# Kernel optimization log

Measured on AMD Instinct MI355X. Metric: run time of the kernel, lower is better.

The kernel has to match this reference:

```python
import jax, jax.numpy as jnp
import numpy as np
from jax import lax

B, T, D = 1, 2048, 2048
H, KVH, HD = 16, 4, 128
BETA = 0.9
ROPE_BASE = 10000.0


def _causal_prefix_ema(x, beta):
    # x: (B, T, D); m_t = beta * m_{t-1} + (1 - beta) * x_t, m_{-1} = 0
    def step(m, xt):
        m = beta * m + (1.0 - beta) * xt
        return m, m
    _, ys = lax.scan(step, jnp.zeros_like(x[:, 0]), jnp.swapaxes(x, 0, 1))
    return jnp.swapaxes(ys, 0, 1)


def _rotate_half(x):
    x1, x2 = jnp.split(x, 2, axis=-1)
    return jnp.concatenate([-x2, x1], axis=-1)


def _rope_cos_sin(t, hd, dtype):
    inv_freq = 1.0 / (ROPE_BASE ** (jnp.arange(0, hd, 2, dtype=jnp.float32) / hd))
    freqs = jnp.arange(t, dtype=jnp.float32)[:, None] * inv_freq[None, :]  # (T, HD/2)
    emb = jnp.concatenate([freqs, freqs], axis=-1)  # (T, HD)
    return jnp.cos(emb).astype(dtype)[None, None], jnp.sin(emb).astype(dtype)[None, None]


def setup_inputs() -> dict:
    key = jax.random.key(0)
    ks = jax.random.split(key, 8)
    std = 0.02
    return {
        "hidden_states": jax.random.normal(ks[0], (B, T, D), jnp.float32),
        "Wq": jax.random.normal(ks[1], (D, H * HD), jnp.float32) * std,
        "Wk": jax.random.normal(ks[2], (D, KVH * HD), jnp.float32) * std,
        "Wv": jax.random.normal(ks[3], (D, KVH * HD), jnp.float32) * std,
        "Wo": jax.random.normal(ks[4], (H * HD, D), jnp.float32) * std,
        "Wr1": jax.random.normal(ks[5], (D, D // 2), jnp.float32) * std,
        "br1": jnp.zeros((D // 2,), jnp.float32),
        "Wr2": jax.random.normal(ks[6], (D // 2, 2), jnp.float32) * std,
        "br2": jnp.zeros((2,), jnp.float32),
    }


def reference(hidden_states, Wq, Wk, Wv, Wo, Wr1, br1, Wr2, br2):
    b, t, d = hidden_states.shape
    q = hidden_states @ Wq  # (B, T, H*HD)

    # multi-level memories: l1 = raw, l2 = causal prefix EMA
    l2 = _causal_prefix_ema(hidden_states, BETA)

    # router MLP on q + softmax over levels
    h = jax.nn.silu(q @ Wr1 + br1)
    lam = jax.nn.softmax(h @ Wr2 + br2, axis=-1)  # (B, T, 2)
    fused = lam[..., 0:1] * hidden_states + lam[..., 1:2] * l2

    # shape to heads
    q_s = q.reshape(b, t, H, HD).transpose(0, 2, 1, 3)                 # (B, H, T, HD)
    k_s = (fused @ Wk).reshape(b, t, KVH, HD).transpose(0, 2, 1, 3)    # (B, KVH, T, HD)
    v_s = (fused @ Wv).reshape(b, t, KVH, HD).transpose(0, 2, 1, 3)

    # RoPE
    cos, sin = _rope_cos_sin(t, HD, q_s.dtype)
    q_s = q_s * cos + _rotate_half(q_s) * sin
    k_s = k_s * cos + _rotate_half(k_s) * sin

    # repeat kv for GQA
    n_rep = H // KVH
    k_s = jnp.repeat(k_s, n_rep, axis=1)
    v_s = jnp.repeat(v_s, n_rep, axis=1)

    # causal SDPA
    scale = 1.0 / jnp.sqrt(jnp.asarray(HD, q_s.dtype))
    scores = jnp.einsum("bhqd,bhkd->bhqk", q_s, k_s) * scale
    causal = jnp.tril(jnp.ones((t, t), dtype=bool))
    scores = jnp.where(causal[None, None], scores, jnp.finfo(scores.dtype).min)
    attn = jax.nn.softmax(scores, axis=-1)
    out = jnp.einsum("bhqk,bhkd->bhqd", attn, v_s)  # (B, H, T, HD)

    out = out.transpose(0, 2, 1, 3).reshape(b, t, H * HD)
    return out @ Wo
```

## Files before the change

### kernel.cpp

```cpp
#include <hip/hip_runtime.h>
#include <hip/hip_bf16.h>

#define T_SEQ 2048
#define D_MODEL 2048
#define NH 16
#define NKVH 4
#define HD 128

typedef __attribute__((ext_vector_type(8))) short bf16x8;
typedef __attribute__((ext_vector_type(4))) float f32x4;

static __device__ __forceinline__ short f32_to_bf16(float f) {
    unsigned u = __float_as_uint(f);
    u += 0x7fffu + ((u >> 16) & 1u);
    return (short)(u >> 16);
}
static __device__ __forceinline__ float bf16_to_f32(short s) {
    return __uint_as_float(((unsigned)(unsigned short)s) << 16);
}
static __device__ __forceinline__ void gl_to_lds16(const void* g, void* l) {
    __builtin_amdgcn_global_load_lds(
        (const __attribute__((address_space(1))) unsigned int*)g,
        (__attribute__((address_space(3))) unsigned int*)l, 16, 0, 0);
}

template<int BM>
__global__ __launch_bounds__(256) void gemm_bt_kernel(
    const short* __restrict__ A, const short* __restrict__ Bt,
    float* __restrict__ Cf, short* __restrict__ Cb,
    int M, int N, int K, const float* __restrict__ bias, int act)
{
    constexpr int NI = (BM == 128) ? 4 : 2;
    constexpr int ACH = BM / 32;
    __shared__ short Alds[2][BM * 64];
    __shared__ short Blds[2][128 * 64];

    const int tid = threadIdx.x;
    const int wave = tid >> 6, lane = tid & 63;
    const int l16 = lane & 15, quad = lane >> 4;
    const int wm = (BM == 128) ? (wave >> 1) * 64 : 0;
    const int wn = (BM == 128) ? (wave & 1) * 64 : wave * 32;
    const int m0 = blockIdx.y * BM, n0 = blockIdx.x * 128;
    const int niter = K >> 6;

    f32x4 acc[4][NI] = {};

    #pragma unroll
    for (int p = 0; p < ACH; ++p) {
        int li = p * 256 + tid;
        int row = li >> 3, sc = li & 7;
        gl_to_lds16(A + (size_t)(m0 + row) * K + ((sc ^ (row & 7)) * 8),
                    &Alds[0][(size_t)(p * 256 + wave * 64) * 8]);
    }
    #pragma unroll
    for (int p = 0; p < 4; ++p) {
        int li = p * 256 + tid;
        int row = li >> 3, sc = li & 7;
        gl_to_lds16(Bt + (size_t)(n0 + row) * K + ((sc ^ (row & 7)) * 8),
                    &Blds[0][(size_t)(p * 256 + wave * 64) * 8]);
    }

    for (int t = 0; t < niter; ++t) {
        asm volatile("s_waitcnt vmcnt(0)\n\ts_barrier" ::: "memory");

        if (t + 1 < niter) {
            int k1 = (t + 1) << 6;
            int nb = (t + 1) & 1;
            #pragma unroll
            for (int p = 0; p < ACH; ++p) {
                int li = p * 256 + tid;
                int row = li >> 3, sc = li & 7;
                gl_to_lds16(A + (size_t)(m0 + row) * K + k1 + ((sc ^ (row & 7)) * 8),
                            &Alds[nb][(size_t)(p * 256 + wave * 64) * 8]);
            }
            #pragma unroll
            for (int p = 0; p < 4; ++p) {
                int li = p * 256 + tid;
                int row = li >> 3, sc = li & 7;
                gl_to_lds16(Bt + (size_t)(n0 + row) * K + k1 + ((sc ^ (row & 7)) * 8),
                            &Blds[nb][(size_t)(p * 256 + wave * 64) * 8]);
            }
        }

        const short* Ab = Alds[t & 1];
        const short* Bb = Blds[t & 1];
        #pragma unroll
        for (int kk = 0; kk < 2; ++kk) {
            bf16x8 a[4], b[NI];
            #pragma unroll
            for (int i = 0; i < 4; ++i)
                a[i] = *(const bf16x8*)
                    &Ab[(size_t)(wm + i * 16 + l16) * 64 + (((kk * 4 + quad) ^ (l16 & 7)) * 8)];
            #pragma unroll
            for (int i = 0; i < NI; ++i)
                b[i] = *(const bf16x8*)
                    &Bb[(size_t)(wn + i * 16 + l16) * 64 + (((kk * 4 + quad) ^ (l16 & 7)) * 8)];
            #pragma unroll
            for (int mi = 0; mi < 4; ++mi)
                #pragma unroll
                for (int ni = 0; ni < NI; ++ni)
                    acc[mi][ni] = __builtin_amdgcn_mfma_f32_16x16x32_bf16(
                        a[mi], b[ni], acc[mi][ni], 0, 0, 0);
        }
    }

    #pragma unroll
    for (int mi = 0; mi < 4; ++mi) {
        #pragma unroll
        for (int ni = 0; ni < NI; ++ni) {
            int col = n0 + wn + ni * 16 + l16;
            float bv = bias ? bias[col] : 0.0f;
            #pragma unroll
            for (int r = 0; r < 4; ++r) {
                int row = m0 + wm + mi * 16 + quad * 4 + r;
                float x = acc[mi][ni][r] + bv;
                if (act) x = x / (1.0f + __expf(-x));
                size_t o = (size_t)row * N + col;
                if (Cf) Cf[o] = x;
                if (Cb) Cb[o] = f32_to_bf16(x);
            }
        }
    }
}

__global__ __launch_bounds__(256) void transpose_all_kernel(
    const float* __restrict__ Wq, const float* __restrict__ Wk,
    const float* __restrict__ Wv, const float* __restrict__ Wr1,
    const float* __restrict__ Wo, short* __restrict__ Wq_t,
    short* __restrict__ Wkv_t, short* __restrict__ Wr1_t,
    short* __restrict__ Wo_t)
{
    __shared__ float tile[32][33];
    int bx = blockIdx.x;
    const float* src; short* dst; int ld, cb;
    if (bx < 64)       { src = Wq;  dst = Wq_t;  ld = 2048; cb = bx; }
    else if (bx < 80)  { src = Wk;  dst = Wkv_t; ld = 512;  cb = bx - 64; }
    else if (bx < 96)  { src = Wv;  dst = Wkv_t + (size_t)512 * 2048; ld = 512; cb = bx - 80; }
    else if (bx < 128) { src = Wr1; dst = Wr1_t; ld = 1024; cb = bx - 96; }
    else               { src = Wo;  dst = Wo_t;  ld = 2048; cb = bx - 128; }
    int c0 = cb * 32, r0 = blockIdx.y * 32;
    int t = threadIdx.x;
    int r = t >> 3, c4 = (t & 7) * 4;
    float4 v = *(const float4*)&src[(size_t)(r0 + r) * ld + c0 + c4];
    tile[r][c4 + 0] = v.x; tile[r][c4 + 1] = v.y;
    tile[r][c4 + 2] = v.z; tile[r][c4 + 3] = v.w;
    __syncthreads();
    short o[4];
    #pragma unroll
    for (int j = 0; j < 4; ++j) o[j] = f32_to_bf16(tile[c4 + j][r]);
    *(uint2*)&dst[(size_t)(c0 + r) * 2048 + r0 + c4] = *(const uint2*)o;
}

__global__ __launch_bounds__(256) void transpose_bf_kernel(
    const short* __restrict__ src, int ld, short* __restrict__ dst, int ldd)
{
    __shared__ float tile[32][33];
    int r0 = blockIdx.y * 32, c0 = blockIdx.x * 32;
    int x = threadIdx.x & 31, y = threadIdx.x >> 5;
    #pragma unroll
    for (int i = 0; i < 4; ++i)
        tile[y + i * 8][x] = bf16_to_f32(src[(size_t)(r0 + y + i * 8) * ld + c0 + x]);
    __syncthreads();
    #pragma unroll
    for (int i = 0; i < 4; ++i)
        dst[(size_t)(c0 + y + i * 8) * ldd + r0 + x] = f32_to_bf16(tile[x][y + i * 8]);
}

__global__ void conv_bf16_kernel(const float* __restrict__ src, short* __restrict__ dst)
{
    int i = blockIdx.x * blockDim.x + threadIdx.x;
    float4 v = ((const float4*)src)[i];
    short o[4] = {f32_to_bf16(v.x), f32_to_bf16(v.y), f32_to_bf16(v.z), f32_to_bf16(v.w)};
    *(uint2*)(dst + (size_t)i * 4) = *(const uint2*)o;
}

__global__ __launch_bounds__(256) void ema_kernel(const float* __restrict__ hs,
                                                  float* __restrict__ l2)
{
    int d = blockIdx.y * 256 + threadIdx.x;
    int t0 = blockIdx.x * 128;
    int ts = t0 - 192; if (ts < 0) ts = 0;
    float m = 0.0f;
    for (int tb = ts; tb < t0; tb += 16) {
        float buf[16];
        #pragma unroll
        for (int j = 0; j < 16; ++j) buf[j] = hs[(size_t)(tb + j) * D_MODEL + d];
        #pragma unroll
        for (int j = 0; j < 16; ++j) m = 0.9f * m + 0.1f * buf[j];
    }
    for (int tb = t0; tb < t0 + 128; tb += 16) {
        float buf[16];
        #pragma unroll
        for (int j = 0; j < 16; ++j) buf[j] = hs[(size_t)(tb + j) * D_MODEL + d];
        #pragma unroll
        for (int j = 0; j < 16; ++j) { m = 0.9f * m + 0.1f * buf[j]; buf[j] = m; }
        #pragma unroll
        for (int j = 0; j < 16; ++j) l2[(size_t)(tb + j) * D_MODEL + d] = buf[j];
    }
}

__global__ __launch_bounds__(64) void lam_kernel(
    const short* __restrict__ h, const float* __restrict__ Wr2,
    const float* __restrict__ br2, float* __restrict__ lam)
{
    int t = blockIdx.x;
    int lane = threadIdx.x;
    float z0 = 0.0f, z1 = 0.0f;
    for (int i = lane; i < 1024; i += 64) {
        float hv = bf16_to_f32(h[(size_t)t * 1024 + i]);
        z0 += hv * Wr2[i * 2 + 0];
        z1 += hv * Wr2[i * 2 + 1];
    }
    #pragma unroll
    for (int off = 1; off < 64; off <<= 1) {
        z0 += __shfl_xor(z0, off);
        z1 += __shfl_xor(z1, off);
    }
    if (lane == 0) {
        z0 += br2[0]; z1 += br2[1];
        float mx = fmaxf(z0, z1);
        float e0 = expf(z0 - mx), e1 = expf(z1 - mx);
        float inv = 1.0f / (e0 + e1);
        lam[t * 2 + 0] = e0 * inv;
        lam[t * 2 + 1] = e1 * inv;
    }
}

__global__ void fuse_kernel(const float* __restrict__ hs, const float* __restrict__ l2,
                            const float* __restrict__ lam, short* __restrict__ fused)
{
    int idx = blockIdx.x * blockDim.x + threadIdx.x;
    int t = idx >> 9;
    float a0 = lam[t * 2 + 0], a1 = lam[t * 2 + 1];
    float4 a = ((const float4*)hs)[idx];
    float4 b = ((const float4*)l2)[idx];
    short o[4] = {f32_to_bf16(a0 * a.x + a1 * b.x), f32_to_bf16(a0 * a.y + a1 * b.y),
                  f32_to_bf16(a0 * a.z + a1 * b.z), f32_to_bf16(a0 * a.w + a1 * b.w)};
    *(uint2*)(fused + (size_t)idx * 4) = *(const uint2*)o;
}

__global__ void rope_q_kernel(const short* __restrict__ q, short* __restrict__ qr)
{
    int idx = blockIdx.x * blockDim.x + threadIdx.x;
    int d = idx & 63;
    int h = (idx >> 6) & 15;
    int t = idx >> 10;
    float fr = (float)t * __expf(-(float)d * 0.14391156831212787f);
    float s, c;
    sincosf(fr, &s, &c);
    const float sc = 0.08838834764831845f;
    const short* src = q + (size_t)t * D_MODEL + h * HD;
    float x1 = bf16_to_f32(src[d]) * sc, x2 = bf16_to_f32(src[d + 64]) * sc;
    short* dst = qr + ((size_t)h * T_SEQ + t) * HD;
    dst[d]      = f32_to_bf16(x1 * c - x2 * s);
    dst[d + 64] = f32_to_bf16(x2 * c + x1 * s);
}

__global__ void rope_k_kernel(const short* __restrict__ kv, short* __restrict__ kr)
{
    int idx = blockIdx.x * blockDim.x + threadIdx.x;
    int d = idx & 63;
    int kh = (idx >> 6) & 3;
    int t = idx >> 8;
    float fr = (float)t * __expf(-(float)d * 0.14391156831212787f);
    float s, c;
    sincosf(fr, &s, &c);
    const short* src = kv + (size_t)t * 1024 + kh * HD;
    float x1 = bf16_to_f32(src[d]), x2 = bf16_to_f32(src[d + 64]);
    short* dst = kr + ((size_t)kh * T_SEQ + t) * HD;
    dst[d]      = f32_to_bf16(x1 * c - x2 * s);
    dst[d + 64] = f32_to_bf16(x2 * c + x1 * s);
}

__global__ __launch_bounds__(256, 1) void attn_kernel(
    const short* __restrict__ Qr, const short* __restrict__ Kr,
    const short* __restrict__ Vt, short* __restrict__ Out)
{
    const int pi = blockIdx.x;
    const int h = blockIdx.y;
    const int kvh = h >> 2;
    const int tid = threadIdx.x;
    const int wave = tid >> 6, lane = tid & 63;
    const int l16 = lane & 15, quad = lane >> 4;

    __shared__ short Klds[2][128 * 128];
    __shared__ short Vlds[2][128 * 128];
    __shared__ short Plds[4][16][136];

    const short* kbase = Kr + (size_t)kvh * T_SEQ * HD;
    const short* vbase = Vt + (size_t)kvh * HD * T_SEQ;

    for (int ph = 0; ph < 2; ++ph) {
        const int qt = ph ? (31 - pi) : pi;
        const int qbase = qt * 64 + wave * 16;
        const int n = (qt * 64 + 191) >> 7;

        bf16x8 qf[4];
        {
            const short* qrow = Qr + ((size_t)h * T_SEQ + qbase + l16) * HD;
            #pragma unroll
            for (int kc = 0; kc < 4; ++kc)
                qf[kc] = *(const bf16x8*)&qrow[kc * 32 + quad * 8];
        }
        f32x4 o[8] = {};
        float lsum[4] = {0.0f, 0.0f, 0.0f, 0.0f};

        __syncthreads();

        {
            const short* ks = kbase;
            #pragma unroll
            for (int p = 0; p < 8; ++p) {
                int li = p * 256 + tid;
                int row = li >> 4, gs = (li & 15) ^ (row & 15);
                gl_to_lds16(ks + (size_t)row * HD + gs * 8,
                            &Klds[0][(size_t)(p * 256 + wave * 64) * 8]);
            }
            #pragma unroll
            for (int p = 0; p < 8; ++p) {
                int li = p * 256 + tid;
                int row = li >> 4, gs = (li & 15) ^ (row & 15);
                gl_to_lds16(vbase + (size_t)row * T_SEQ + gs * 8,
                            &Vlds[0][(size_t)(p * 256 + wave * 64) * 8]);
            }
        }

        for (int t = 0; t < n; ++t) {
            asm volatile("s_waitcnt vmcnt(0)\n\ts_barrier" ::: "memory");

            if (t + 1 < n) {
                int kv1 = (t + 1) << 7;
                int nb = (t + 1) & 1;
                const short* ks = kbase + (size_t)kv1 * HD;
                #pragma unroll
                for (int p = 0; p < 8; ++p) {
                    int li = p * 256 + tid;
                    int row = li >> 4, gs = (li & 15) ^ (row & 15);
                    gl_to_lds16(ks + (size_t)row * HD + gs * 8,
                                &Klds[nb][(size_t)(p * 256 + wave * 64) * 8]);
                }
                #pragma unroll
                for (int p = 0; p < 8; ++p) {
                    int li = p * 256 + tid;
                    int row = li >> 4, gs = (li & 15) ^ (row & 15);
                    gl_to_lds16(vbase + (size_t)row * T_SEQ + kv1 + gs * 8,
                                &Vlds[nb][(size_t)(p * 256 + wave * 64) * 8]);
                }
            }

            const short* Kb = Klds[t & 1];
            const short* Vb = Vlds[t & 1];

            f32x4 s[8];
            #pragma unroll
            for (int ni = 0; ni < 8; ++ni) s[ni] = (f32x4){0, 0, 0, 0};
            #pragma unroll
            for (int ni = 0; ni < 8; ++ni)
                #pragma unroll
                for (int kc = 0; kc < 4; ++kc) {
                    bf16x8 b = *(const bf16x8*)
                        &Kb[(size_t)(ni * 16 + l16) * 128 + (((kc * 4 + quad) ^ l16) * 8)];
                    s[ni] = __builtin_amdgcn_mfma_f32_16x16x32_bf16(qf[kc], b, s[ni], 0, 0, 0);
                }

            if (t == n - 1) {
                int kvg0 = t << 7;
                #pragma unroll
                for (int ni = 0; ni < 8; ++ni) {
                    int kvg = kvg0 + ni * 16 + l16;
                    #pragma unroll
                    for (int r = 0; r < 4; ++r) {
                        int qg = qbase + quad * 4 + r;
                        float p = (kvg <= qg) ? __expf(s[ni][r]) : 0.0f;
                        lsum[r] += p;
                        Plds[wave][quad * 4 + r][ni * 16 + l16] = f32_to_bf16(p);
                    }
                }
            } else {
                #pragma unroll
                for (int ni = 0; ni < 8; ++ni)
                    #pragma unroll
                    for (int r = 0; r < 4; ++r) {
                        float p = __expf(s[ni][r]);
                        lsum[r] += p;
                        Plds[wave][quad * 4 + r][ni * 16 + l16] = f32_to_bf16(p);
                    }
            }
            asm volatile("s_waitcnt lgkmcnt(0)" ::: "memory");

            #pragma unroll
            for (int kc = 0; kc < 4; ++kc) {
                bf16x8 pa = *(const bf16x8*)&Plds[wave][l16][kc * 32 + quad * 8];
                #pragma unroll
                for (int d8 = 0; d8 < 8; ++d8) {
                    bf16x8 b = *(const bf16x8*)
                        &Vb[(size_t)(d8 * 16 + l16) * 128 + (((kc * 4 + quad) ^ l16) * 8)];
                    o[d8] = __builtin_amdgcn_mfma_f32_16x16x32_bf16(pa, b, o[d8], 0, 0, 0);
                }
            }
        }

        #pragma unroll
        for (int r = 0; r < 4; ++r) {
            #pragma unroll
            for (int off = 1; off < 16; off <<= 1)
                lsum[r] += __shfl_xor(lsum[r], off);
            lsum[r] = 1.0f / lsum[r];
        }
        #pragma unroll
        for (int d8 = 0; d8 < 8; ++d8)
            #pragma unroll
            for (int r = 0; r < 4; ++r) {
                int row = qbase + quad * 4 + r;
                Out[(size_t)row * D_MODEL + h * HD + d8 * 16 + l16] =
                    f32_to_bf16(o[d8][r] * lsum[r]);
            }
    }
}

extern "C" void kernel_launch(void* const* d_in, const int* in_sizes, int n_in,
                              void* d_out, int out_size, void* d_ws, size_t ws_size,
                              hipStream_t stream)
{
    const float* hs  = (const float*)d_in[0];
    const float* Wq  = (const float*)d_in[1];
    const float* Wk  = (const float*)d_in[2];
    const float* Wv  = (const float*)d_in[3];
    const float* Wo  = (const float*)d_in[4];
    const float* Wr1 = (const float*)d_in[5];
    const float* br1 = (const float*)d_in[6];
    const float* Wr2 = (const float*)d_in[7];
    const float* br2 = (const float*)d_in[8];
    float* out = (float*)d_out;

    char* w = (char*)d_ws;
    const size_t MB = 1u << 20;
    float* l2_f     = (float*)(w + 0 * MB);
    short* hs_bf    = (short*)(w + 16 * MB);
    short* Wq_t     = (short*)(w + 24 * MB);
    short* Wkv_t    = (short*)(w + 32 * MB);
    short* Wr1_t    = (short*)(w + 36 * MB);
    short* Wo_t     = (short*)(w + 40 * MB);
    short* q_bf     = (short*)(w + 48 * MB);
    short* h_bf     = (short*)(w + 56 * MB);
    short* fused_bf = (short*)(w + 60 * MB);
    short* kv_bf    = (short*)(w + 68 * MB);
    short* qr       = (short*)(w + 72 * MB);
    short* kr       = (short*)(w + 80 * MB);
    short* vr       = (short*)(w + 82 * MB);
    float* lam_f    = (float*)(w + 84 * MB);
    short* attn_bf  = hs_bf;

    transpose_all_kernel<<<dim3(192, 64), 256, 0, stream>>>(
        Wq, Wk, Wv, Wr1, Wo, Wq_t, Wkv_t, Wr1_t, Wo_t);
    conv_bf16_kernel<<<(T_SEQ * D_MODEL / 4) / 256, 256, 0, stream>>>(hs, hs_bf);

    ema_kernel<<<dim3(T_SEQ / 128, D_MODEL / 256), 256, 0, stream>>>(hs, l2_f);

    gemm_bt_kernel<128><<<dim3(16, 16), 256, 0, stream>>>(
        hs_bf, Wq_t, nullptr, q_bf, 2048, 2048, 2048, nullptr, 0);

    gemm_bt_kernel<64><<<dim3(8, 32), 256, 0, stream>>>(
        q_bf, Wr1_t, nullptr, h_bf, 2048, 1024, 2048, br1, 1);

    lam_kernel<<<T_SEQ, 64, 0, stream>>>(h_bf, Wr2, br2, lam_f);

    fuse_kernel<<<(T_SEQ * D_MODEL / 4) / 256, 256, 0, stream>>>(hs, l2_f, lam_f, fused_bf);

    gemm_bt_kernel<64><<<dim3(8, 32), 256, 0, stream>>>(
        fused_bf, Wkv_t, nullptr, kv_bf, 2048, 1024, 2048, nullptr, 0);

    rope_q_kernel<<<(T_SEQ * NH * 64) / 256, 256, 0, stream>>>(q_bf, qr);
    rope_k_kernel<<<(T_SEQ * NKVH * 64) / 256, 256, 0, stream>>>(kv_bf, kr);
    transpose_bf_kernel<<<dim3(16, 64), 256, 0, stream>>>(kv_bf + 512, 1024, vr, 2048);

    attn_kernel<<<dim3(16, NH), 256, 0, stream>>>(qr, kr, vr, attn_bf);

    gemm_bt_kernel<128><<<dim3(16, 16), 256, 0, stream>>>(
        attn_bf, Wo_t, out, nullptr, 2048, 2048, 2048, nullptr, 0);
}
```

Before: 349.5 us.

## Retile attention to 128-row query blocks and fuse bf16 conversion into EMA

The attention kernel drops the two-phase paired query tiles. Each block now processes one 128-row query tile, with each wave owning 32 rows as two MFMA sub-tiles. KV tiles are reduced to 64 rows, and P is staged in a shared swizzled LDS buffer, so K/V fragments are reused across two query sub-tiles. The hidden-state fp32-to-bf16 conversion is folded into the EMA kernel, removing a separate pass over the input. Without the tile pairing, causal work per block becomes imbalanced, which may leave late blocks as stragglers.

```diff
diff --git a/kernel.cpp b/kernel.cpp
--- a/kernel.cpp
+++ b/kernel.cpp
@@ -166,16 +166,9 @@
         dst[(size_t)(c0 + y + i * 8) * ldd + r0 + x] = f32_to_bf16(tile[x][y + i * 8]);
 }
 
-__global__ void conv_bf16_kernel(const float* __restrict__ src, short* __restrict__ dst)
-{
-    int i = blockIdx.x * blockDim.x + threadIdx.x;
-    float4 v = ((const float4*)src)[i];
-    short o[4] = {f32_to_bf16(v.x), f32_to_bf16(v.y), f32_to_bf16(v.z), f32_to_bf16(v.w)};
-    *(uint2*)(dst + (size_t)i * 4) = *(const uint2*)o;
-}
-
 __global__ __launch_bounds__(256) void ema_kernel(const float* __restrict__ hs,
-                                                  float* __restrict__ l2)
+                                                  float* __restrict__ l2,
+                                                  short* __restrict__ hs_b)
 {
     int d = blockIdx.y * 256 + threadIdx.x;
     int t0 = blockIdx.x * 128;
@@ -192,6 +185,8 @@
         float buf[16];
         #pragma unroll
         for (int j = 0; j < 16; ++j) buf[j] = hs[(size_t)(tb + j) * D_MODEL + d];
+        #pragma unroll
+        for (int j = 0; j < 16; ++j) hs_b[(size_t)(tb + j) * D_MODEL + d] = f32_to_bf16(buf[j]);
         #pragma unroll
         for (int j = 0; j < 16; ++j) { m = 0.9f * m + 0.1f * buf[j]; buf[j] = m; }
         #pragma unroll
@@ -276,146 +271,171 @@
     const short* __restrict__ Qr, const short* __restrict__ Kr,
     const short* __restrict__ Vt, short* __restrict__ Out)
 {
-    const int pi = blockIdx.x;
+    const int qt = blockIdx.x;
     const int h = blockIdx.y;
     const int kvh = h >> 2;
     const int tid = threadIdx.x;
     const int wave = tid >> 6, lane = tid & 63;
     const int l16 = lane & 15, quad = lane >> 4;
 
-    __shared__ short Klds[2][128 * 128];
-    __shared__ short Vlds[2][128 * 128];
-    __shared__ short Plds[4][16][136];
+    __shared__ short Klds[2][64 * 128];
+    __shared__ short Vlds[2][128 * 64];
+    __shared__ short Plds[128 * 64];
 
     const short* kbase = Kr + (size_t)kvh * T_SEQ * HD;
     const short* vbase = Vt + (size_t)kvh * HD * T_SEQ;
-
-    for (int ph = 0; ph < 2; ++ph) {
-        const int qt = ph ? (31 - pi) : pi;
-        const int qbase = qt * 64 + wave * 16;
-        const int n = (qt * 64 + 191) >> 7;
-
-        bf16x8 qf[4];
-        {
-            const short* qrow = Qr + ((size_t)h * T_SEQ + qbase + l16) * HD;
-            #pragma unroll
-            for (int kc = 0; kc < 4; ++kc)
-                qf[kc] = *(const bf16x8*)&qrow[kc * 32 + quad * 8];
-        }
-        f32x4 o[8] = {};
-        float lsum[4] = {0.0f, 0.0f, 0.0f, 0.0f};
-
-        __syncthreads();
-
-        {
-            const short* ks = kbase;
-            #pragma unroll
-            for (int p = 0; p < 8; ++p) {
+    const int qblk = qt * 128;
+    const int qrow0 = qblk + wave * 32;
+    const int n = 2 * qt + 2;
+
+    bf16x8 qf[2][4];
+    #pragma unroll
+    for (int qs = 0; qs < 2; ++qs) {
+        const short* qrow = Qr + ((size_t)h * T_SEQ + qrow0 + qs * 16 + l16) * HD;
+        #pragma unroll
+        for (int kc = 0; kc < 4; ++kc)
+            qf[qs][kc] = *(const bf16x8*)&qrow[kc * 32 + quad * 8];
+    }
+    f32x4 o[2][8] = {};
+    float lsum[2][4] = {};
+
+    #pragma unroll
+    for (int p = 0; p < 4; ++p) {
+        int li = p * 256 + tid;
+        int row = li >> 4, gs = (li & 15) ^ (row & 15);
+        gl_to_lds16(kbase + (size_t)row * HD + gs * 8,
+                    &Klds[0][(size_t)(p * 256 + wave * 64) * 8]);
+    }
+    #pragma unroll
+    for (int p = 0; p < 4; ++p) {
+        int li = p * 256 + tid;
+        int row = li >> 3, gs = (li & 7) ^ (row & 7);
+        gl_to_lds16(vbase + (size_t)row * T_SEQ + gs * 8,
+                    &Vlds[0][(size_t)(p * 256 + wave * 64) * 8]);
+    }
+
+    for (int t = 0; t < n; ++t) {
+        asm volatile("s_waitcnt vmcnt(0)\n\ts_barrier" ::: "memory");
+
+        if (t + 1 < n) {
+            int kv1 = (t + 1) << 6;
+            int nb = (t + 1) & 1;
+            const short* ks = kbase + (size_t)kv1 * HD;
+            #pragma unroll
+            for (int p = 0; p < 4; ++p) {
                 int li = p * 256 + tid;
                 int row = li >> 4, gs = (li & 15) ^ (row & 15);
                 gl_to_lds16(ks + (size_t)row * HD + gs * 8,
-                            &Klds[0][(size_t)(p * 256 + wave * 64) * 8]);
-            }
-            #pragma unroll
-            for (int p = 0; p < 8; ++p) {
+                            &Klds[nb][(size_t)(p * 256 + wave * 64) * 8]);
+            }
+            #pragma unroll
+            for (int p = 0; p < 4; ++p) {
                 int li = p * 256 + tid;
-                int row = li >> 4, gs = (li & 15) ^ (row & 15);
-                gl_to_lds16(vbase + (size_t)row * T_SEQ + gs * 8,
-                            &Vlds[0][(size_t)(p * 256 + wave * 64) * 8]);
+                int row = li >> 3, gs = (li & 7) ^ (row & 7);
+                gl_to_lds16(vbase + (size_t)row * T_SEQ + kv1 + gs * 8,
+                            &Vlds[nb][(size_t)(p * 256 + wave * 64) * 8]);
             }
         }
 
-        for (int t = 0; t < n; ++t) {
-            asm volatile("s_waitcnt vmcnt(0)\n\ts_barrier" ::: "memory");
-
-            if (t + 1 < n) {
-                int kv1 = (t + 1) << 7;
-                int nb = (t + 1) & 1;
-                const short* ks = kbase + (size_t)kv1 * HD;
-                #pragma unroll
-                for (int p = 0; p < 8; ++p) {
-                    int li = p * 256 + tid;
-                    int row = li >> 4, gs = (li & 15) ^ (row & 15);
-                    gl_to_lds16(ks + (size_t)row * HD + gs * 8,
-                                &Klds[nb][(size_t)(p * 256 + wave * 64) * 8]);
-                }
-                #pragma unroll
-                for (int p = 0; p < 8; ++p) {
-                    int li = p * 256 + tid;
-                    int row = li >> 4, gs = (li & 15) ^ (row & 15);
-                    gl_to_lds16(vbase + (size_t)row * T_SEQ + kv1 + gs * 8,
-                                &Vlds[nb][(size_t)(p * 256 + wave * 64) * 8]);
-                }
-            }
-
+        const int kv0 = t << 6;
+        if (qrow0 + 31 >= kv0) {
             const short* Kb = Klds[t & 1];
             const short* Vb = Vlds[t & 1];
 
-            f32x4 s[8];
-            #pragma unroll
-            for (int ni = 0; ni < 8; ++ni) s[ni] = (f32x4){0, 0, 0, 0};
-            #pragma unroll
-            for (int ni = 0; ni < 8; ++ni)
+            f32x4 s[2][4];
+            #pragma unroll
+            for (int qs = 0; qs < 2; ++qs)
+                #pragma unroll
+                for (int ni = 0; ni < 4; ++ni) s[qs][ni] = (f32x4){0, 0, 0, 0};
+            #pragma unroll
+            for (int ni = 0; ni < 4; ++ni)
                 #pragma unroll
                 for (int kc = 0; kc < 4; ++kc) {
+                    int row = ni * 16 + l16;
                     bf16x8 b = *(const bf16x8*)
-                        &Kb[(size_t)(ni * 16 + l16) * 128 + (((kc * 4 + quad) ^ l16) * 8)];
-                    s[ni] = __builtin_amdgcn_mfma_f32_16x16x32_bf16(qf[kc], b, s[ni], 0, 0, 0);
+                        &Kb[(size_t)row * 128 + (((kc * 4 + quad) ^ (row & 15)) * 8)];
+                    #pragma unroll
+                    for (int qs = 0; qs < 2; ++qs)
+                        s[qs][ni] = __builtin_amdgcn_mfma_f32_16x16x32_bf16(
+                            qf[qs][kc], b, s[qs][ni], 0, 0, 0);
                 }
 
-            if (t == n - 1) {
-                int kvg0 = t << 7;
-                #pragma unroll
-                for (int ni = 0; ni < 8; ++ni) {
-                    int kvg = kvg0 + ni * 16 + l16;
+            if (t >= n - 2) {
+                #pragma unroll
+                for (int ni = 0; ni < 4; ++ni) {
+                    int kvg = kv0 + ni * 16 + l16;
                     #pragma unroll
-                    for (int r = 0; r < 4; ++r) {
-                        int qg = qbase + quad * 4 + r;
-                        float p = (kvg <= qg) ? __expf(s[ni][r]) : 0.0f;
-                        lsum[r] += p;
-                        Plds[wave][quad * 4 + r][ni * 16 + l16] = f32_to_bf16(p);
-                    }
+                    for (int qs = 0; qs < 2; ++qs)
+                        #pragma unroll
+                        for (int r = 0; r < 4; ++r) {
+                            int pr = wave * 32 + qs * 16 + quad * 4 + r;
+                            int qg = qblk + pr;
+                            float p = (kvg <= qg) ? __expf(s[qs][ni][r]) : 0.0f;
+                            lsum[qs][r] += p;
+                            int col = ni * 16 + l16;
+                            Plds[pr * 64 + (((col >> 3) ^ (pr & 7)) * 8) + (col & 7)]
+                                = f32_to_bf16(p);
+                        }
                 }
             } else {
                 #pragma unroll
-                for (int ni = 0; ni < 8; ++ni)
+                for (int ni = 0; ni < 4; ++ni)
                     #pragma unroll
-                    for (int r = 0; r < 4; ++r) {
-                        float p = __expf(s[ni][r]);
-                        lsum[r] += p;
-                        Plds[wave][quad * 4 + r][ni * 16 + l16] = f32_to_bf16(p);
-                    }
+                    for (int qs = 0; qs < 2; ++qs)
+                        #pragma unroll
+                        for (int r = 0; r < 4; ++r) {
+                            int pr = wave * 32 + qs * 16 + quad * 4 + r;
+                            float p = __expf(s[qs][ni][r]);
+                            lsum[qs][r] += p;
+                            int col = ni * 16 + l16;
+                            Plds[pr * 64 + (((col >> 3) ^ (pr & 7)) * 8) + (col & 7)]
+                                = f32_to_bf16(p);
+                        }
             }
             asm volatile("s_waitcnt lgkmcnt(0)" ::: "memory");
 
             #pragma unroll
-            for (int kc = 0; kc < 4; ++kc) {
-                bf16x8 pa = *(const bf16x8*)&Plds[wave][l16][kc * 32 + quad * 8];
+            for (int kc2 = 0; kc2 < 2; ++kc2) {
+                bf16x8 pa[2];
+                #pragma unroll
+                for (int qs = 0; qs < 2; ++qs) {
+                    int prow = wave * 32 + qs * 16 + l16;
+                    pa[qs] = *(const bf16x8*)
+                        &Plds[prow * 64 + (((kc2 * 4 + quad) ^ (prow & 7)) * 8)];
+                }
                 #pragma unroll
                 for (int d8 = 0; d8 < 8; ++d8) {
+                    int vrow = d8 * 16 + l16;
                     bf16x8 b = *(const bf16x8*)
-                        &Vb[(size_t)(d8 * 16 + l16) * 128 + (((kc * 4 + quad) ^ l16) * 8)];
-                    o[d8] = __builtin_amdgcn_mfma_f32_16x16x32_bf16(pa, b, o[d8], 0, 0, 0);
+                        &Vb[(size_t)vrow * 64 + (((kc2 * 4 + quad) ^ (vrow & 7)) * 8)];
+                    #pragma unroll
+                    for (int qs = 0; qs < 2; ++qs)
+                        o[qs][d8] = __builtin_amdgcn_mfma_f32_16x16x32_bf16(
+                            pa[qs], b, o[qs][d8], 0, 0, 0);
                 }
             }
         }
-
+    }
+
+    #pragma unroll
+    for (int qs = 0; qs < 2; ++qs)
         #pragma unroll
         for (int r = 0; r < 4; ++r) {
             #pragma unroll
             for (int off = 1; off < 16; off <<= 1)
-                lsum[r] += __shfl_xor(lsum[r], off);
-            lsum[r] = 1.0f / lsum[r];
+                lsum[qs][r] += __shfl_xor(lsum[qs][r], off);
+            lsum[qs][r] = 1.0f / lsum[qs][r];
         }
+    #pragma unroll
+    for (int qs = 0; qs < 2; ++qs)
         #pragma unroll
         for (int d8 = 0; d8 < 8; ++d8)
             #pragma unroll
             for (int r = 0; r < 4; ++r) {
-                int row = qbase + quad * 4 + r;
+                int row = qrow0 + qs * 16 + quad * 4 + r;
                 Out[(size_t)row * D_MODEL + h * HD + d8 * 16 + l16] =
-                    f32_to_bf16(o[d8][r] * lsum[r]);
-            }
-    }
+                    f32_to_bf16(o[qs][d8][r] * lsum[qs][r]);
+            }
 }
 
 extern "C" void kernel_launch(void* const* d_in, const int* in_sizes, int n_in,
@@ -453,9 +473,8 @@
 
     transpose_all_kernel<<<dim3(192, 64), 256, 0, stream>>>(
         Wq, Wk, Wv, Wr1, Wo, Wq_t, Wkv_t, Wr1_t, Wo_t);
-    conv_bf16_kernel<<<(T_SEQ * D_MODEL / 4) / 256, 256, 0, stream>>>(hs, hs_bf);
-
-    ema_kernel<<<dim3(T_SEQ / 128, D_MODEL / 256), 256, 0, stream>>>(hs, l2_f);
+
+    ema_kernel<<<dim3(T_SEQ / 128, D_MODEL / 256), 256, 0, stream>>>(hs, l2_f, hs_bf);
 
     gemm_bt_kernel<128><<<dim3(16, 16), 256, 0, stream>>>(
         hs_bf, Wq_t, nullptr, q_bf, 2048, 2048, 2048, nullptr, 0);
```

Result: slower. 386.3 us (+10.5%).

## Triple-buffer GEMM and attention loads, shrink KV tile, fuse bf16 cast into EMA

Applied to the files above, without the earlier changes.

The GEMM kernel moves from double to triple buffering, issuing loads two K-steps ahead and waiting only on the older stage with partial vmcnt. The attention kernel drops its KV tile from 128 to 64 rows, also triple-buffers through a shared staging helper, and sizes the trip count to the causal extent at 64-row granularity. The standalone fp32-to-bf16 conversion of hidden_states is folded into the EMA kernel, removing one launch and one read pass. These changes target global-load latency stalls and masked work, at the cost of more LDS per block and more loop iterations with barriers in attention.

```diff
diff --git a/kernel.cpp b/kernel.cpp
--- a/kernel.cpp
+++ b/kernel.cpp
@@ -32,8 +32,8 @@
 {
     constexpr int NI = (BM == 128) ? 4 : 2;
     constexpr int ACH = BM / 32;
-    __shared__ short Alds[2][BM * 64];
-    __shared__ short Blds[2][128 * 64];
+    __shared__ short Alds[3][BM * 64];
+    __shared__ short Blds[3][128 * 64];
 
     const int tid = threadIdx.x;
     const int wave = tid >> 6, lane = tid & 63;
@@ -46,26 +46,35 @@
     f32x4 acc[4][NI] = {};
 
     #pragma unroll
-    for (int p = 0; p < ACH; ++p) {
-        int li = p * 256 + tid;
-        int row = li >> 3, sc = li & 7;
-        gl_to_lds16(A + (size_t)(m0 + row) * K + ((sc ^ (row & 7)) * 8),
-                    &Alds[0][(size_t)(p * 256 + wave * 64) * 8]);
-    }
-    #pragma unroll
-    for (int p = 0; p < 4; ++p) {
-        int li = p * 256 + tid;
-        int row = li >> 3, sc = li & 7;
-        gl_to_lds16(Bt + (size_t)(n0 + row) * K + ((sc ^ (row & 7)) * 8),
-                    &Blds[0][(size_t)(p * 256 + wave * 64) * 8]);
+    for (int b0 = 0; b0 < 2; ++b0) {
+        int kb = b0 << 6;
+        #pragma unroll
+        for (int p = 0; p < ACH; ++p) {
+            int li = p * 256 + tid;
+            int row = li >> 3, sc = li & 7;
+            gl_to_lds16(A + (size_t)(m0 + row) * K + kb + ((sc ^ (row & 7)) * 8),
+                        &Alds[b0][(size_t)(p * 256 + wave * 64) * 8]);
+        }
+        #pragma unroll
+        for (int p = 0; p < 4; ++p) {
+            int li = p * 256 + tid;
+            int row = li >> 3, sc = li & 7;
+            gl_to_lds16(Bt + (size_t)(n0 + row) * K + kb + ((sc ^ (row & 7)) * 8),
+                        &Blds[b0][(size_t)(p * 256 + wave * 64) * 8]);
+        }
     }
 
     for (int t = 0; t < niter; ++t) {
-        asm volatile("s_waitcnt vmcnt(0)\n\ts_barrier" ::: "memory");
-
         if (t + 1 < niter) {
-            int k1 = (t + 1) << 6;
-            int nb = (t + 1) & 1;
+            if (BM == 128) asm volatile("s_waitcnt vmcnt(8)\n\ts_barrier" ::: "memory");
+            else           asm volatile("s_waitcnt vmcnt(6)\n\ts_barrier" ::: "memory");
+        } else {
+            asm volatile("s_waitcnt vmcnt(0)\n\ts_barrier" ::: "memory");
+        }
+
+        if (t + 2 < niter) {
+            int k1 = (t + 2) << 6;
+            int nb = (t + 2) % 3;
             #pragma unroll
             for (int p = 0; p < ACH; ++p) {
                 int li = p * 256 + tid;
@@ -82,8 +91,8 @@
             }
         }
 
-        const short* Ab = Alds[t & 1];
-        const short* Bb = Blds[t & 1];
+        const short* Ab = Alds[t % 3];
+        const short* Bb = Blds[t % 3];
         #pragma unroll
         for (int kk = 0; kk < 2; ++kk) {
             bf16x8 a[4], b[NI];
@@ -166,16 +175,9 @@
         dst[(size_t)(c0 + y + i * 8) * ldd + r0 + x] = f32_to_bf16(tile[x][y + i * 8]);
 }
 
-__global__ void conv_bf16_kernel(const float* __restrict__ src, short* __restrict__ dst)
-{
-    int i = blockIdx.x * blockDim.x + threadIdx.x;
-    float4 v = ((const float4*)src)[i];
-    short o[4] = {f32_to_bf16(v.x), f32_to_bf16(v.y), f32_to_bf16(v.z), f32_to_bf16(v.w)};
-    *(uint2*)(dst + (size_t)i * 4) = *(const uint2*)o;
-}
-
 __global__ __launch_bounds__(256) void ema_kernel(const float* __restrict__ hs,
-                                                  float* __restrict__ l2)
+                                                  float* __restrict__ l2,
+                                                  short* __restrict__ hs_b)
 {
     int d = blockIdx.y * 256 + threadIdx.x;
     int t0 = blockIdx.x * 128;
@@ -192,6 +194,8 @@
         float buf[16];
         #pragma unroll
         for (int j = 0; j < 16; ++j) buf[j] = hs[(size_t)(tb + j) * D_MODEL + d];
+        #pragma unroll
+        for (int j = 0; j < 16; ++j) hs_b[(size_t)(tb + j) * D_MODEL + d] = f32_to_bf16(buf[j]);
         #pragma unroll
         for (int j = 0; j < 16; ++j) { m = 0.9f * m + 0.1f * buf[j]; buf[j] = m; }
         #pragma unroll
@@ -272,6 +276,27 @@
     dst[d + 64] = f32_to_bf16(x2 * c + x1 * s);
 }
 
+static __device__ __forceinline__ void attn_stage(
+    const short* kbase, const short* vbase, int kv0,
+    short* Kb, short* Vb, int tid, int wave)
+{
+    const short* ks = kbase + (size_t)kv0 * HD;
+    #pragma unroll
+    for (int p = 0; p < 4; ++p) {
+        int li = p * 256 + tid;
+        int row = li >> 4, gs = (li & 15) ^ (row & 15);
+        gl_to_lds16(ks + (size_t)row * HD + gs * 8,
+                    Kb + (size_t)(p * 256 + wave * 64) * 8);
+    }
+    #pragma unroll
+    for (int p = 0; p < 4; ++p) {
+        int li = p * 256 + tid;
+        int row = li >> 3, gs = (li & 7) ^ (row & 7);
+        gl_to_lds16(vbase + (size_t)row * T_SEQ + kv0 + gs * 8,
+                    Vb + (size_t)(p * 256 + wave * 64) * 8);
+    }
+}
+
 __global__ __launch_bounds__(256, 1) void attn_kernel(
     const short* __restrict__ Qr, const short* __restrict__ Kr,
     const short* __restrict__ Vt, short* __restrict__ Out)
@@ -283,9 +308,9 @@
     const int wave = tid >> 6, lane = tid & 63;
     const int l16 = lane & 15, quad = lane >> 4;
 
-    __shared__ short Klds[2][128 * 128];
-    __shared__ short Vlds[2][128 * 128];
-    __shared__ short Plds[4][16][136];
+    __shared__ short Klds[3][64 * 128];
+    __shared__ short Vlds[3][128 * 64];
+    __shared__ short Plds[4][16][72];
 
     const short* kbase = Kr + (size_t)kvh * T_SEQ * HD;
     const short* vbase = Vt + (size_t)kvh * HD * T_SEQ;
@@ -293,7 +318,7 @@
     for (int ph = 0; ph < 2; ++ph) {
         const int qt = ph ? (31 - pi) : pi;
         const int qbase = qt * 64 + wave * 16;
-        const int n = (qt * 64 + 191) >> 7;
+        const int n = qt + 1;
 
         bf16x8 qf[4];
         {
@@ -307,66 +332,39 @@
 
         __syncthreads();
 
-        {
-            const short* ks = kbase;
-            #pragma unroll
-            for (int p = 0; p < 8; ++p) {
-                int li = p * 256 + tid;
-                int row = li >> 4, gs = (li & 15) ^ (row & 15);
-                gl_to_lds16(ks + (size_t)row * HD + gs * 8,
-                            &Klds[0][(size_t)(p * 256 + wave * 64) * 8]);
-            }
-            #pragma unroll
-            for (int p = 0; p < 8; ++p) {
-                int li = p * 256 + tid;
-                int row = li >> 4, gs = (li & 15) ^ (row & 15);
-                gl_to_lds16(vbase + (size_t)row * T_SEQ + gs * 8,
-                            &Vlds[0][(size_t)(p * 256 + wave * 64) * 8]);
-            }
-        }
+        attn_stage(kbase, vbase, 0, Klds[0], Vlds[0], tid, wave);
+        if (n > 1) attn_stage(kbase, vbase, 64, Klds[1], Vlds[1], tid, wave);
 
         for (int t = 0; t < n; ++t) {
-            asm volatile("s_waitcnt vmcnt(0)\n\ts_barrier" ::: "memory");
-
-            if (t + 1 < n) {
-                int kv1 = (t + 1) << 7;
-                int nb = (t + 1) & 1;
-                const short* ks = kbase + (size_t)kv1 * HD;
-                #pragma unroll
-                for (int p = 0; p < 8; ++p) {
-                    int li = p * 256 + tid;
-                    int row = li >> 4, gs = (li & 15) ^ (row & 15);
-                    gl_to_lds16(ks + (size_t)row * HD + gs * 8,
-                                &Klds[nb][(size_t)(p * 256 + wave * 64) * 8]);
-                }
-                #pragma unroll
-                for (int p = 0; p < 8; ++p) {
-                    int li = p * 256 + tid;
-                    int row = li >> 4, gs = (li & 15) ^ (row & 15);
-                    gl_to_lds16(vbase + (size_t)row * T_SEQ + kv1 + gs * 8,
-                                &Vlds[nb][(size_t)(p * 256 + wave * 64) * 8]);
-                }
-            }
-
-            const short* Kb = Klds[t & 1];
-            const short* Vb = Vlds[t & 1];
-
-            f32x4 s[8];
-            #pragma unroll
-            for (int ni = 0; ni < 8; ++ni) s[ni] = (f32x4){0, 0, 0, 0};
-            #pragma unroll
-            for (int ni = 0; ni < 8; ++ni)
+            if (t + 1 < n)
+                asm volatile("s_waitcnt vmcnt(8)\n\ts_barrier" ::: "memory");
+            else
+                asm volatile("s_waitcnt vmcnt(0)\n\ts_barrier" ::: "memory");
+
+            if (t + 2 < n)
+                attn_stage(kbase, vbase, (t + 2) << 6,
+                           Klds[(t + 2) % 3], Vlds[(t + 2) % 3], tid, wave);
+
+            const short* Kb = Klds[t % 3];
+            const short* Vb = Vlds[t % 3];
+
+            f32x4 s[4];
+            #pragma unroll
+            for (int ni = 0; ni < 4; ++ni) s[ni] = (f32x4){0, 0, 0, 0};
+            #pragma unroll
+            for (int ni = 0; ni < 4; ++ni)
                 #pragma unroll
                 for (int kc = 0; kc < 4; ++kc) {
+                    int row = ni * 16 + l16;
                     bf16x8 b = *(const bf16x8*)
-                        &Kb[(size_t)(ni * 16 + l16) * 128 + (((kc * 4 + quad) ^ l16) * 8)];
+                        &Kb[(size_t)row * 128 + (((kc * 4 + quad) ^ (row & 15)) * 8)];
                     s[ni] = __builtin_amdgcn_mfma_f32_16x16x32_bf16(qf[kc], b, s[ni], 0, 0, 0);
                 }
 
             if (t == n - 1) {
-                int kvg0 = t << 7;
+                int kvg0 = t << 6;
                 #pragma unroll
-                for (int ni = 0; ni < 8; ++ni) {
+                for (int ni = 0; ni < 4; ++ni) {
                     int kvg = kvg0 + ni * 16 + l16;
                     #pragma unroll
                     for (int r = 0; r < 4; ++r) {
@@ -378,7 +376,7 @@
                 }
             } else {
                 #pragma unroll
-                for (int ni = 0; ni < 8; ++ni)
+                for (int ni = 0; ni < 4; ++ni)
                     #pragma unroll
                     for (int r = 0; r < 4; ++r) {
                         float p = __expf(s[ni][r]);
@@ -389,12 +387,13 @@
             asm volatile("s_waitcnt lgkmcnt(0)" ::: "memory");
 
             #pragma unroll
-            for (int kc = 0; kc < 4; ++kc) {
-                bf16x8 pa = *(const bf16x8*)&Plds[wave][l16][kc * 32 + quad * 8];
+            for (int kc2 = 0; kc2 < 2; ++kc2) {
+                bf16x8 pa = *(const bf16x8*)&Plds[wave][l16][kc2 * 32 + quad * 8];
                 #pragma unroll
                 for (int d8 = 0; d8 < 8; ++d8) {
+                    int vrow = d8 * 16 + l16;
                     bf16x8 b = *(const bf16x8*)
-                        &Vb[(size_t)(d8 * 16 + l16) * 128 + (((kc * 4 + quad) ^ l16) * 8)];
+                        &Vb[(size_t)vrow * 64 + (((kc2 * 4 + quad) ^ (vrow & 7)) * 8)];
                     o[d8] = __builtin_amdgcn_mfma_f32_16x16x32_bf16(pa, b, o[d8], 0, 0, 0);
                 }
             }
@@ -453,9 +452,8 @@
 
     transpose_all_kernel<<<dim3(192, 64), 256, 0, stream>>>(
         Wq, Wk, Wv, Wr1, Wo, Wq_t, Wkv_t, Wr1_t, Wo_t);
-    conv_bf16_kernel<<<(T_SEQ * D_MODEL / 4) / 256, 256, 0, stream>>>(hs, hs_bf);
-
-    ema_kernel<<<dim3(T_SEQ / 128, D_MODEL / 256), 256, 0, stream>>>(hs, l2_f);
+
+    ema_kernel<<<dim3(T_SEQ / 128, D_MODEL / 256), 256, 0, stream>>>(hs, l2_f, hs_bf);
 
     gemm_bt_kernel<128><<<dim3(16, 16), 256, 0, stream>>>(
         hs_bf, Wq_t, nullptr, q_bf, 2048, 2048, 2048, nullptr, 0);
```

Result: slower. 361.2 us (+3.4%).
